# Performance work log

Measured on AMD Instinct MI355X. Metric: run time of the kernel, lower is better.

Reference implementation:

```python
import jax, jax.numpy as jnp
import numpy as np

P = 100000   # num places
T = 100000   # num transitions
E = 400000   # edges per direction
H = 128      # hidden_dim
L = 3        # num_gnn_layers


def setup_inputs() -> dict:
    key = jax.random.key(0)
    ks = jax.random.split(key, 24)
    w = lambda i, sh: jax.random.normal(ks[i], sh, dtype=jnp.float32) * 0.02
    z = lambda sh: jnp.zeros(sh, dtype=jnp.float32)
    return {
        "place_features": jax.random.uniform(ks[0], (P,), dtype=jnp.float32),
        "transition_features": jax.random.normal(ks[1], (T, 8), dtype=jnp.float32),
        "prefix_encoding": jax.random.normal(ks[2], (18,), dtype=jnp.float32),
        # pre edges: place -> transition ; post edges: transition -> place
        "pre_edge_index": jnp.stack([jax.random.randint(ks[3], (E,), 0, P),
                                     jax.random.randint(ks[4], (E,), 0, T)]).astype(jnp.int32),
        "post_edge_index": jnp.stack([jax.random.randint(ks[5], (E,), 0, T),
                                      jax.random.randint(ks[6], (E,), 0, P)]).astype(jnp.int32),
        # embeddings
        "W_pe": w(7, (1, H)), "b_pe": z((H,)),
        "W_te": w(8, (8, H)), "b_te": z((H,)),
        "W_pr": w(9, (18, H)), "b_pr": z((H,)),
        # per-layer HeteroGraphConv params (stacked over L)
        "p2t_W": w(10, (L, H, H)), "p2t_b": z((L, H)),
        "t2p_W": w(11, (L, H, H)), "t2p_b": z((L, H)),
        "pu_W": w(12, (L, 2 * H, H)), "pu_b": z((L, H)),
        "tu_W": w(13, (L, 2 * H, H)), "tu_b": z((L, H)),
        "pa_W": w(14, (L, H)), "pa_b": z((L,)),
        "ta_W": w(15, (L, H)), "ta_b": z((L,)),
        # pooling + predictor head
        "W_pp": w(16, (H, H)), "b_pp": z((H,)),
        "W_tp": w(17, (H, H)), "b_tp": z((H,)),
        "W1": w(18, (3 * H, 2 * H)), "b1": z((2 * H,)),
        "W2": w(19, (2 * H, H)), "b2": z((H,)),
        "W3": w(20, (H, T)), "b3": z((T,)),
    }


def _forward(place_features, transition_features, prefix_encoding,
             W_pe, b_pe, W_te, b_te, W_pr, b_pr,
             p2t_W, p2t_b, t2p_W, t2p_b, pu_W, pu_b, tu_W, tu_b,
             pa_W, pa_b, ta_W, ta_b,
             W_pp, b_pp, W_tp, b_tp, W1, b1, W2, b2, W3, b3,
             pre_edge_index, post_edge_index):
    place_h = place_features[:, None] @ W_pe + b_pe            # [P,H]
    trans_h = transition_features @ W_te + b_te                # [T,H]
    prefix_h = prefix_encoding[None, :] @ W_pr + b_pr          # [1,H]
    p_src, p_dst = pre_edge_index[0], pre_edge_index[1]        # place idx, trans idx
    t_src, t_dst = post_edge_index[0], post_edge_index[1]      # trans idx, place idx
    nP, nT = place_h.shape[0], trans_h.shape[0]
    for l in range(L):  # fixed small layer count
        # place -> transition: gather, linear, softmax over ALL edges (dim=0 in torch), scatter-add
        m_pt = place_h[p_src] @ p2t_W[l] + p2t_b[l]            # [E,H]
        a_pt = jax.nn.softmax(m_pt @ ta_W[l] + ta_b[l], axis=0)  # [E]
        trans_msg = jax.ops.segment_sum(m_pt * a_pt[:, None], p_dst, num_segments=nT)
        # transition -> place
        m_tp = trans_h[t_src] @ t2p_W[l] + t2p_b[l]            # [E,H]
        a_tp = jax.nn.softmax(m_tp @ pa_W[l] + pa_b[l], axis=0)
        place_msg = jax.ops.segment_sum(m_tp * a_tp[:, None], t_dst, num_segments=nP)
        # residual update + relu (dropout is identity at eval)
        place_new = jnp.concatenate([place_h, place_msg], axis=1) @ pu_W[l] + pu_b[l]
        trans_new = jnp.concatenate([trans_h, trans_msg], axis=1) @ tu_W[l] + tu_b[l]
        place_h = jax.nn.relu(place_h + place_new)
        trans_h = jax.nn.relu(trans_h + trans_new)
    place_global = jnp.mean(place_h @ W_pp + b_pp, axis=0, keepdims=True)   # [1,H]
    trans_global = jnp.mean(trans_h @ W_tp + b_tp, axis=0, keepdims=True)   # [1,H]
    combined = jnp.concatenate([place_global, trans_global, prefix_h], axis=1)  # [1,3H]
    h1 = jax.nn.relu(combined @ W1 + b1)
    h2 = jax.nn.relu(h1 @ W2 + b2)
    logits = h2 @ W3 + b3                                      # [1,T]
    return jax.nn.sigmoid(logits)                              # predicted_transitions


def reference(place_features, transition_features, prefix_encoding,
              pre_edge_index, post_edge_index,
              W_pe, b_pe, W_te, b_te, W_pr, b_pr,
              p2t_W, p2t_b, t2p_W, t2p_b, pu_W, pu_b, tu_W, tu_b,
              pa_W, pa_b, ta_W, ta_b,
              W_pp, b_pp, W_tp, b_tp, W1, b1, W2, b2, W3, b3):
    return _forward(place_features, transition_features, prefix_encoding,
                    W_pe, b_pe, W_te, b_te, W_pr, b_pr,
                    p2t_W, p2t_b, t2p_W, t2p_b, pu_W, pu_b, tu_W, tu_b,
                    pa_W, pa_b, ta_W, ta_b,
                    W_pp, b_pp, W_tp, b_tp, W1, b1, W2, b2, W3, b3,
                    pre_edge_index, post_edge_index)
```

## Files before the change

### kernel.cpp

```cpp
#include <hip/hip_runtime.h>
#include <cstddef>

#define H 128

typedef unsigned short ushort_t;
typedef unsigned char uchar_t;
typedef __attribute__((ext_vector_type(8))) short short8;
typedef __attribute__((ext_vector_type(4))) float floatx4;
typedef __attribute__((ext_vector_type(2))) float floatx2;

__device__ __forceinline__ unsigned fkey(float f){
    unsigned u = __float_as_uint(f);
    return (u & 0x80000000u) ? ~u : (u | 0x80000000u);
}
__device__ __forceinline__ float funkey(unsigned k){
    unsigned u = (k & 0x80000000u) ? (k ^ 0x80000000u) : ~k;
    return __uint_as_float(u);
}
__device__ __forceinline__ ushort_t f2bf(float f){
    unsigned u = __float_as_uint(f);
    u += 0x7fffu + ((u >> 16) & 1u);
    return (ushort_t)(u >> 16);
}
__device__ __forceinline__ float bf2f(ushort_t h){
    return __uint_as_float(((unsigned)h) << 16);
}
__device__ __forceinline__ uchar_t f2fp8(float v){
    int p = __builtin_amdgcn_cvt_pk_fp8_f32(v, v, 0, false);
    return (uchar_t)(p & 0xff);
}
__device__ __forceinline__ void gll16(const void* g, void* l){
    __builtin_amdgcn_global_load_lds(
        (const __attribute__((address_space(1))) unsigned int*)g,
        (__attribute__((address_space(3))) unsigned int*)l, 16, 0, 0);
}

__global__ __launch_bounds__(256) void k_embed_place(
    const float* __restrict__ pf, const float* __restrict__ Wpe,
    const float* __restrict__ bpe, ushort_t* __restrict__ out, int P)
{
    int idx = blockIdx.x*256 + threadIdx.x;
    if (idx >= P*32) return;
    int p = idx >> 5, q = (idx & 31) << 2;
    float v = pf[p];
    float4 w = *(const float4*)(Wpe + q);
    float4 b = *(const float4*)(bpe + q);
    ushort4 o;
    o.x = f2bf(v*w.x + b.x); o.y = f2bf(v*w.y + b.y);
    o.z = f2bf(v*w.z + b.z); o.w = f2bf(v*w.w + b.w);
    *(ushort4*)(out + (size_t)p*H + q) = o;
}

__global__ __launch_bounds__(256) void k_embed_trans(
    const float* __restrict__ tf, const float* __restrict__ Wte,
    const float* __restrict__ bte, ushort_t* __restrict__ out, int T)
{
    __shared__ float Wl[8*H];
    __shared__ float Bl[H];
    int tid = threadIdx.x;
    #pragma unroll
    for (int t = 0; t < 4; t++) Wl[tid + t*256] = Wte[tid + t*256];
    if (tid < H) Bl[tid] = bte[tid];
    __syncthreads();
    int idx = blockIdx.x*256 + tid;
    if (idx >= T*32) return;
    int t = idx >> 5, q = (idx & 31) << 2;
    float4 acc = *(float4*)(&Bl[q]);
    #pragma unroll
    for (int k = 0; k < 8; k++){
        float s = tf[(size_t)t*8 + k];
        float4 w = *(float4*)(&Wl[k*H + q]);
        acc.x += s*w.x; acc.y += s*w.y; acc.z += s*w.z; acc.w += s*w.w;
    }
    ushort4 o;
    o.x = f2bf(acc.x); o.y = f2bf(acc.y); o.z = f2bf(acc.z); o.w = f2bf(acc.w);
    *(ushort4*)(out + (size_t)t*H + q) = o;
}

__global__ void k_init_small(const float* __restrict__ pe, int plen,
                             const float* __restrict__ Wpr, const float* __restrict__ bpr,
                             float* __restrict__ prefix, float* __restrict__ meanP,
                             float* __restrict__ meanT, float* __restrict__ slots)
{
    int c = threadIdx.x;
    float a = bpr[c];
    for (int k = 0; k < plen; k++) a += pe[k]*Wpr[k*H + c];
    prefix[c] = a;
    meanP[c] = 0.f;
    meanT[c] = 0.f;
    if (c < 16) slots[c] = 0.f;
}

__global__ __launch_bounds__(256) void k_wconv(
    const float* __restrict__ p2t_W, const float* __restrict__ t2p_W,
    const float* __restrict__ tu_W,  const float* __restrict__ pu_W,
    ushort_t* __restrict__ WT, int total)
{
    int e = blockIdx.x*256 + threadIdx.x;
    if (e >= total) return;
    int l = e / 98304, o = e - l*98304;
    const float* src; int K, oo;
    if (o < 16384)      { src = p2t_W + (size_t)l*16384; K = 128; oo = o; }
    else if (o < 32768) { src = t2p_W + (size_t)l*16384; K = 128; oo = o - 16384; }
    else if (o < 65536) { src = tu_W  + (size_t)l*32768; K = 256; oo = o - 32768; }
    else                { src = pu_W  + (size_t)l*32768; K = 256; oo = o - 65536; }
    int n = oo / K, k = oo - n*K;
    WT[e] = f2bf(src[(size_t)k*H + n]);
}

__global__ __launch_bounds__(256) void k_zero_ints(int* __restrict__ p, int n)
{
    int i = blockIdx.x*256 + threadIdx.x;
    int stride = gridDim.x*256;
    for (; i < n; i += stride) p[i] = 0;
}

__global__ __launch_bounds__(256) void k_hist2(
    const int* __restrict__ preD, const int* __restrict__ postD, int E,
    int* __restrict__ cntPre, int* __restrict__ cntPost,
    int* __restrict__ rankPre, int* __restrict__ rankPost)
{
    int i = blockIdx.x*256 + threadIdx.x;
    int stride = gridDim.x*256;
    for (; i < E; i += stride){
        rankPre[i] = atomicAdd(&cntPre[preD[i]], 1);
        rankPost[i] = atomicAdd(&cntPost[postD[i]], 1);
    }
}

__global__ __launch_bounds__(256) void k_scan_part(
    const int* __restrict__ cnt, int N, int* __restrict__ bsum)
{
    __shared__ int wsum[4];
    int tid = threadIdx.x, lane = tid & 63, wid = tid >> 6;
    int base = blockIdx.x*1024 + tid*4;
    int4 v = make_int4(0,0,0,0);
    if (base + 3 < N) v = *(const int4*)(cnt + base);
    else {
        if (base+0 < N) v.x = cnt[base+0];
        if (base+1 < N) v.y = cnt[base+1];
        if (base+2 < N) v.z = cnt[base+2];
    }
    int s = v.x + v.y + v.z + v.w;
    #pragma unroll
    for (int o = 1; o < 64; o <<= 1) s += __shfl_xor(s, o);
    if (lane == 0) wsum[wid] = s;
    __syncthreads();
    if (tid == 0) bsum[blockIdx.x] = wsum[0] + wsum[1] + wsum[2] + wsum[3];
}

__global__ __launch_bounds__(256) void k_scan_bsum(int* __restrict__ bsum, int nb)
{
    __shared__ int wsum[4];
    int tid = threadIdx.x, lane = tid & 63, wid = tid >> 6;
    int x = (tid < nb) ? bsum[tid] : 0;
    int inc = x;
    #pragma unroll
    for (int o = 1; o < 64; o <<= 1){
        int u = __shfl_up(inc, o);
        if (lane >= o) inc += u;
    }
    if (lane == 63) wsum[wid] = inc;
    __syncthreads();
    int woff = 0;
    if (wid > 0) woff += wsum[0];
    if (wid > 1) woff += wsum[1];
    if (wid > 2) woff += wsum[2];
    if (tid < nb) bsum[tid] = woff + inc - x;
}

__global__ __launch_bounds__(256) void k_scan_final(
    const int* __restrict__ cnt, int N, const int* __restrict__ bsum,
    int* __restrict__ rp, int E)
{
    __shared__ int wsum[4];
    int tid = threadIdx.x, lane = tid & 63, wid = tid >> 6;
    int base = blockIdx.x*1024 + tid*4;
    int4 v = make_int4(0,0,0,0);
    if (base + 3 < N) v = *(const int4*)(cnt + base);
    else {
        if (base+0 < N) v.x = cnt[base+0];
        if (base+1 < N) v.y = cnt[base+1];
        if (base+2 < N) v.z = cnt[base+2];
    }
    int t0 = v.x, t1 = t0 + v.y, t2 = t1 + v.z, t3 = t2 + v.w;
    int inc = t3;
    #pragma unroll
    for (int o = 1; o < 64; o <<= 1){
        int u = __shfl_up(inc, o);
        if (lane >= o) inc += u;
    }
    if (lane == 63) wsum[wid] = inc;
    __syncthreads();
    int woff = 0;
    if (wid > 0) woff += wsum[0];
    if (wid > 1) woff += wsum[1];
    if (wid > 2) woff += wsum[2];
    int off = bsum[blockIdx.x] + woff + inc - t3;
    if (base+0 < N) rp[base+0] = off;
    if (base+1 < N) rp[base+1] = off + t0;
    if (base+2 < N) rp[base+2] = off + t1;
    if (base+3 < N) rp[base+3] = off + t2;
    if (blockIdx.x == 0 && tid == 0) rp[N] = E;
}

__global__ __launch_bounds__(256) void k_fill2(
    const int* __restrict__ preS, const int* __restrict__ preD,
    const int* __restrict__ postS, const int* __restrict__ postD, int E,
    const int* __restrict__ rpPre, const int* __restrict__ rankPre, int* __restrict__ csrPre,
    const int* __restrict__ rpPost, const int* __restrict__ rankPost, int* __restrict__ csrPost)
{
    int i = blockIdx.x*256 + threadIdx.x;
    int stride = gridDim.x*256;
    for (; i < E; i += stride){
        csrPre[rpPre[preD[i]] + rankPre[i]] = preS[i];
        csrPost[rpPost[postD[i]] + rankPost[i]] = postS[i];
    }
}

__global__ __launch_bounds__(256, 4) void k_gemm_msg(
    const ushort_t* __restrict__ A, const ushort_t* __restrict__ WT,
    const float* __restrict__ bias, uchar_t* __restrict__ out, int M,
    const float* __restrict__ aw, float* __restrict__ y4)
{
    __shared__ __align__(16) char As[3*4096];
    int tid = threadIdx.x;
    int lane = tid & 63, wid = tid >> 6;
    int quad = lane >> 4, l15 = lane & 15;
    int strip = wid*32;
    short8 bfr[2][4];
    float bcol[2], awc[2];
    #pragma unroll
    for (int j = 0; j < 2; j++){
        int col = strip + j*16 + l15;
        #pragma unroll
        for (int kk = 0; kk < 4; kk++)
            bfr[j][kk] = *(const short8*)(WT + (size_t)col*128 + kk*32 + quad*8);
        bcol[j] = bias[col];
        awc[j]  = aw[col];
    }
    int tiles = (M + 15) >> 4;
    int G = gridDim.x;
    int t0 = blockIdx.x;
    if (t0 >= tiles) return;

    int srow = tid >> 4;
    int su = (tid & 15) ^ srow;
    const ushort_t* gb = A + (size_t)srow*H + su*8;
    char* AsB = As;

    #define STAGE_MSG(bo, t) gll16(gb + (size_t)(t)*(16*H), AsB + (bo) + (wid<<10))

    STAGE_MSG(0, t0);
    int t1p = t0 + G;
    if (t1p < tiles){
        STAGE_MSG(4096, t1p);
        asm volatile("s_waitcnt vmcnt(1)\ns_barrier" ::: "memory");
    } else {
        asm volatile("s_waitcnt vmcnt(0)\ns_barrier" ::: "memory");
    }

    int t = t0, bo = 0;
    for (;;){
        const char* rb = AsB + bo;
        short8 afr[4];
        #pragma unroll
        for (int kk = 0; kk < 4; kk++)
            afr[kk] = *(const short8*)(rb + (l15<<8) + ((((kk<<2)+quad) ^ l15) << 4));
        floatx4 acc[2];
        acc[0] = (floatx4)0.f; acc[1] = (floatx4)0.f;
        #pragma unroll
        for (int j = 0; j < 2; j++)
            #pragma unroll
            for (int kk = 0; kk < 4; kk++)
                acc[j] = __builtin_amdgcn_mfma_f32_16x16x32_bf16(afr[kk], bfr[j][kk], acc[j], 0,0,0);
        int row0 = t << 4;
        float pr[4] = {0.f,0.f,0.f,0.f};
        #pragma unroll
        for (int j = 0; j < 2; j++){
            int col = strip + j*16 + l15;
            #pragma unroll
            for (int rr = 0; rr < 4; rr++){
                int grow = row0 + quad*4 + rr;
                float v = acc[j][rr] + bcol[j];
                out[(size_t)grow*H + col] = f2fp8(v);
                pr[rr] += v * awc[j];
            }
        }
        #pragma unroll
        for (int rr = 0; rr < 4; rr++){
            float p = pr[rr];
            p += __shfl_xor(p, 1); p += __shfl_xor(p, 2);
            p += __shfl_xor(p, 4); p += __shfl_xor(p, 8);
            int grow = row0 + quad*4 + rr;
            if (l15 == 0) y4[(size_t)grow*4 + wid] = p;
        }
        int tn = t + G;
        if (tn >= tiles) break;
        int tnn = tn + G;
        int bo2 = bo + 4096; if (bo2 >= 12288) bo2 = 0;
        int bo3 = bo2 + 4096; if (bo3 >= 12288) bo3 = 0;
        if (tnn < tiles){
            STAGE_MSG(bo3, tnn);
            asm volatile("s_waitcnt vmcnt(13)\ns_barrier" ::: "memory");
        } else {
            asm volatile("s_waitcnt vmcnt(12)\ns_barrier" ::: "memory");
        }
        t = tn; bo = bo2;
    }
    #undef STAGE_MSG
}

__global__ __launch_bounds__(256) void k_scoremax(
    const float* __restrict__ y4, int N, const float* __restrict__ abp,
    float* __restrict__ y, unsigned* __restrict__ Mkey)
{
    __shared__ float wm[4];
    int tid = threadIdx.x;
    int lane = tid & 63, wid = tid >> 6;
    int gid = blockIdx.x*256 + tid, stride = gridDim.x*256;
    float ab = abp[0];
    float lmax = -3.402823466e38f;
    for (int r = gid; r < N; r += stride){
        float4 v = *(const float4*)(y4 + (size_t)r*4);
        float s = v.x + v.y + v.z + v.w + ab;
        y[r] = s;
        lmax = fmaxf(lmax, s);
    }
    #pragma unroll
    for (int o = 1; o < 64; o <<= 1) lmax = fmaxf(lmax, __shfl_xor(lmax, o));
    if (lane == 0) wm[wid] = lmax;
    __syncthreads();
    if (tid == 0){
        float m = fmaxf(fmaxf(wm[0], wm[1]), fmaxf(wm[2], wm[3]));
        atomicMax(Mkey, fkey(m));
    }
}

__global__ __launch_bounds__(256) void k_sumexp(
    const int* __restrict__ src, int E, const float* __restrict__ y,
    const unsigned* __restrict__ Mkey, float* __restrict__ Sp)
{
    __shared__ float red[4];
    int tid = threadIdx.x, lane = tid & 63, wid = tid >> 6;
    int gid = blockIdx.x*256 + tid, stride = gridDim.x*256;
    float Mv = funkey(Mkey[0]);
    float ls = 0.f;
    for (int e = gid; e < E; e += stride) ls += expf(y[src[e]] - Mv);
    #pragma unroll
    for (int o = 1; o < 64; o <<= 1) ls += __shfl_xor(ls, o);
    if (lane == 0) red[wid] = ls;
    __syncthreads();
    if (tid == 0) atomicAdd(Sp, red[0] + red[1] + red[2] + red[3]);
}

__global__ __launch_bounds__(256, 3) void k_gemm_up(
    const ushort_t* __restrict__ A1, const ushort_t* __restrict__ A2,
    const ushort_t* __restrict__ WT, const float* __restrict__ bias,
    const float* __restrict__ Sp, ushort_t* __restrict__ out, int M,
    float* __restrict__ colsum)
{
    __shared__ __align__(16) char As[3*8192];
    __shared__ float csum[H];
    int tid = threadIdx.x;
    int lane = tid & 63, wid = tid >> 6;
    int quad = lane >> 4, l15 = lane & 15;
    int strip = wid*32;
    short8 bfr1[2][4], bfr2[2][4];
    float bcol[2];
    #pragma unroll
    for (int j = 0; j < 2; j++){
        int col = strip + j*16 + l15;
        #pragma unroll
        for (int kk = 0; kk < 4; kk++){
            bfr1[j][kk] = *(const short8*)(WT + (size_t)col*256 + kk*32 + quad*8);
            bfr2[j][kk] = *(const short8*)(WT + (size_t)col*256 + 128 + kk*32 + quad*8);
        }
        bcol[j] = bias[col];
    }
    short8 If0, If1;
    #pragma unroll
    for (int e = 0; e < 8; e++){
        int kloc = quad*8 + e;
        If0[e] = (kloc == l15)      ? (short)0x3F80 : (short)0;
        If1[e] = (kloc == l15 + 16) ? (short)0x3F80 : (short)0;
    }
    float invS = 1.f / Sp[0];
    const bool has_cs = (colsum != nullptr);
    if (has_cs && tid < H) csum[tid] = 0.f;

    int tiles = (M + 15) >> 4;
    int G = gridDim.x;
    int t0 = blockIdx.x;
    if (t0 >= tiles) return;
    int srow = tid >> 4;
    int su = (tid & 15) ^ srow;
    const ushort_t* g1b = A1 + (size_t)srow*H + su*8;
    const ushort_t* g2b = A2 + (size_t)srow*H + su*8;
    char* AsB = As;

    #define STAGE_UP(bo, t) do { \
        gll16(g1b + (size_t)(t)*(16*H), AsB + (bo) + (wid<<10)); \
        gll16(g2b + (size_t)(t)*(16*H), AsB + (bo) + 4096 + (wid<<10)); \
    } while(0)

    STAGE_UP(0, t0);
    int t1p = t0 + G;
    if (t1p < tiles){
        STAGE_UP(8192, t1p);
        asm volatile("s_waitcnt vmcnt(2)\ns_barrier" ::: "memory");
    } else {
        asm volatile("s_waitcnt vmcnt(0)\ns_barrier" ::: "memory");
    }

    float cs[2] = {0.f, 0.f};
    int t = t0, bo = 0;
    for (;;){
        const char* rb = AsB + bo;
        short8 a1f[4], a2f[4];
        #pragma unroll
        for (int kk = 0; kk < 4; kk++){
            int sw = ((((kk<<2)+quad) ^ l15) << 4);
            a1f[kk] = *(const short8*)(rb + (l15<<8) + sw);
            a2f[kk] = *(const short8*)(rb + 4096 + (l15<<8) + sw);
        }
        short8 ares = *(const short8*)(rb + (l15<<8) + ((((wid<<2)+quad) ^ l15) << 4));
        floatx4 acc1[2], acc2[2];
        acc1[0] = __builtin_amdgcn_mfma_f32_16x16x32_bf16(ares, If0, (floatx4)0.f, 0,0,0);
        acc1[1] = __builtin_amdgcn_mfma_f32_16x16x32_bf16(ares, If1, (floatx4)0.f, 0,0,0);
        acc2[0] = (floatx4)0.f; acc2[1] = (floatx4)0.f;
        #pragma unroll
        for (int j = 0; j < 2; j++){
            #pragma unroll
            for (int kk = 0; kk < 4; kk++)
                acc1[j] = __builtin_amdgcn_mfma_f32_16x16x32_bf16(a1f[kk], bfr1[j][kk], acc1[j], 0,0,0);
            #pragma unroll
            for (int kk = 0; kk < 4; kk++)
                acc2[j] = __builtin_amdgcn_mfma_f32_16x16x32_bf16(a2f[kk], bfr2[j][kk], acc2[j], 0,0,0);
        }
        int row0 = t << 4;
        #pragma unroll
        for (int j = 0; j < 2; j++){
            int col = strip + j*16 + l15;
            #pragma unroll
            for (int rr = 0; rr < 4; rr++){
                int grow = row0 + quad*4 + rr;
                float v = acc1[j][rr] + invS*acc2[j][rr] + bcol[j];
                v = fmaxf(v, 0.f);
                out[(size_t)grow*H + col] = f2bf(v);
                if (has_cs) cs[j] += v;
            }
        }
        int tn = t + G;
        if (tn >= tiles) break;
        int tnn = tn + G;
        int bo2 = bo + 8192; if (bo2 >= 24576) bo2 = 0;
        int bo3 = bo2 + 8192; if (bo3 >= 24576) bo3 = 0;
        if (tnn < tiles){
            STAGE_UP(bo3, tnn);
            asm volatile("s_waitcnt vmcnt(10)\ns_barrier" ::: "memory");
        } else {
            asm volatile("s_waitcnt vmcnt(8)\ns_barrier" ::: "memory");
        }
        t = tn; bo = bo2;
    }
    #undef STAGE_UP
    if (has_cs){
        #pragma unroll
        for (int j = 0; j < 2; j++){
            float v = cs[j];
            v += __shfl_xor(v, 16); v += __shfl_xor(v, 32);
            if (quad == 0) atomicAdd(&csum[strip + j*16 + l15], v);
        }
        __syncthreads();
        if (tid < H) atomicAdd(&colsum[tid], csum[tid]);
    }
}

__device__ __forceinline__ void acc8f8(float* a, int2 u, float w){
    floatx2 p;
    p = __builtin_amdgcn_cvt_pk_f32_fp8(u.x, false); a[0] += w*p.x; a[1] += w*p.y;
    p = __builtin_amdgcn_cvt_pk_f32_fp8(u.x, true);  a[2] += w*p.x; a[3] += w*p.y;
    p = __builtin_amdgcn_cvt_pk_f32_fp8(u.y, false); a[4] += w*p.x; a[5] += w*p.y;
    p = __builtin_amdgcn_cvt_pk_f32_fp8(u.y, true);  a[6] += w*p.x; a[7] += w*p.y;
}

__global__ __launch_bounds__(256) void k_gather(
    const int* __restrict__ rp, const int* __restrict__ csr, int Nrow,
    const float* __restrict__ y, const uchar_t* __restrict__ X,
    ushort_t* __restrict__ Mb, const unsigned* __restrict__ Mkey)
{
    int tid = threadIdx.x;
    int g = tid >> 4, gl = tid & 15;
    int r = blockIdx.x*16 + g;
    if (r >= Nrow) return;
    float Mv = funkey(Mkey[0]);
    int j0 = rp[r], j1 = rp[r+1];
    const int2* X8 = (const int2*)X;
    float a[8] = {0.f,0.f,0.f,0.f,0.f,0.f,0.f,0.f};
    int j = j0;
    for (; j + 1 < j1; j += 2){
        int s0 = csr[j], s1 = csr[j+1];
        float e0 = expf(y[s0] - Mv);
        float e1 = expf(y[s1] - Mv);
        int2 u0 = X8[(size_t)s0*16 + gl];
        int2 u1 = X8[(size_t)s1*16 + gl];
        acc8f8(a, u0, e0);
        acc8f8(a, u1, e1);
    }
    if (j < j1){
        int s0 = csr[j];
        float e0 = expf(y[s0] - Mv);
        int2 u0 = X8[(size_t)s0*16 + gl];
        acc8f8(a, u0, e0);
    }
    int4 o;
    o.x = (int)((((unsigned)f2bf(a[1])) << 16) | (unsigned)f2bf(a[0]));
    o.y = (int)((((unsigned)f2bf(a[3])) << 16) | (unsigned)f2bf(a[2]));
    o.z = (int)((((unsigned)f2bf(a[5])) << 16) | (unsigned)f2bf(a[4]));
    o.w = (int)((((unsigned)f2bf(a[7])) << 16) | (unsigned)f2bf(a[6]));
    ((int4*)Mb)[(size_t)r*16 + gl] = o;
}

__global__ __launch_bounds__(256) void k_head(
    const float* __restrict__ meanP, const float* __restrict__ meanT,
    float invP, float invT,
    const float* __restrict__ Wpp, const float* __restrict__ bpp,
    const float* __restrict__ Wtp, const float* __restrict__ btp,
    const float* __restrict__ prefix,
    const float* __restrict__ W1, const float* __restrict__ b1,
    const float* __restrict__ W2, const float* __restrict__ b2,
    float* __restrict__ h2g)
{
    __shared__ float comb[384];
    __shared__ float h1s[256];
    int tid = threadIdx.x;
    if (tid < 128){
        float a = bpp[tid];
        for (int k = 0; k < 128; k++) a += meanP[k]*invP*Wpp[k*H + tid];
        comb[tid] = a;
        comb[256 + tid] = prefix[tid];
    } else {
        int c = tid - 128;
        float a = btp[c];
        for (int k = 0; k < 128; k++) a += meanT[k]*invT*Wtp[k*H + c];
        comb[128 + c] = a;
    }
    __syncthreads();
    {
        float a = b1[tid];
        for (int k = 0; k < 384; k++) a += comb[k]*W1[k*256 + tid];
        h1s[tid] = fmaxf(a, 0.f);
    }
    __syncthreads();
    if (tid < 128){
        float a = b2[tid];
        for (int k = 0; k < 256; k++) a += h1s[k]*W2[k*H + tid];
        h2g[tid] = fmaxf(a, 0.f);
    }
}

__global__ __launch_bounds__(256) void k_logits(
    const float* __restrict__ h2g, const float* __restrict__ W3,
    const float* __restrict__ b3, float* __restrict__ out, int T)
{
    __shared__ float h2l[128];
    int tid = threadIdx.x;
    if (tid < 128) h2l[tid] = h2g[tid];
    __syncthreads();
    int t = blockIdx.x*256 + tid;
    if (t >= T) return;
    float a = b3[t];
    #pragma unroll 8
    for (int k = 0; k < 128; k++) a += h2l[k]*W3[(size_t)k*T + t];
    out[t] = 1.f/(1.f + expf(-a));
}

extern "C" void kernel_launch(void* const* d_in, const int* in_sizes, int n_in,
                              void* d_out, int out_size, void* d_ws, size_t ws_size,
                              hipStream_t stream)
{
    (void)n_in; (void)out_size; (void)ws_size;
    const float* pf    = (const float*)d_in[0];
    const float* tf    = (const float*)d_in[1];
    const float* pe    = (const float*)d_in[2];
    const int*   pre   = (const int*)d_in[3];
    const int*   post  = (const int*)d_in[4];
    const float* W_pe  = (const float*)d_in[5];
    const float* b_pe  = (const float*)d_in[6];
    const float* W_te  = (const float*)d_in[7];
    const float* b_te  = (const float*)d_in[8];
    const float* W_pr  = (const float*)d_in[9];
    const float* b_pr  = (const float*)d_in[10];
    const float* p2t_W = (const float*)d_in[11];
    const float* p2t_b = (const float*)d_in[12];
    const float* t2p_W = (const float*)d_in[13];
    const float* t2p_b = (const float*)d_in[14];
    const float* pu_W  = (const float*)d_in[15];
    const float* pu_b  = (const float*)d_in[16];
    const float* tu_W  = (const float*)d_in[17];
    const float* tu_b  = (const float*)d_in[18];
    const float* pa_W  = (const float*)d_in[19];
    const float* pa_b  = (const float*)d_in[20];
    const float* ta_W  = (const float*)d_in[21];
    const float* ta_b  = (const float*)d_in[22];
    const float* W_pp  = (const float*)d_in[23];
    const float* b_pp  = (const float*)d_in[24];
    const float* W_tp  = (const float*)d_in[25];
    const float* b_tp  = (const float*)d_in[26];
    const float* W1    = (const float*)d_in[27];
    const float* b1    = (const float*)d_in[28];
    const float* W2    = (const float*)d_in[29];
    const float* b2    = (const float*)d_in[30];
    const float* W3    = (const float*)d_in[31];
    const float* b3    = (const float*)d_in[32];

    int P = in_sizes[0];
    int T = in_sizes[1] / 8;
    int E = in_sizes[3] / 2;
    int plen = in_sizes[2];
    int L = in_sizes[11] / (H*H);

    float* ws = (float*)d_ws;
    size_t fP = (size_t)P*H, fT = (size_t)T*H;
    size_t fN = (fP > fT) ? fP : fT;
    int   Nmax = (P > T) ? P : T;

    float* yb = ws;
    float* y4 = yb + Nmax;
    float* sc = y4 + (size_t)Nmax*4;
    float* meanP   = sc + 16;
    float* meanT   = sc + 144;
    float* prefix  = sc + 272;
    float* h2g     = sc + 400;

    ushort_t* bh = (ushort_t*)(sc + 544);
    ushort_t* place_h = bh;
    ushort_t* trans_h = place_h + fP;
    ushort_t* Mb      = trans_h + fT;
    ushort_t* Pb2     = Mb + fN;
    ushort_t* Tb2     = Pb2 + fP;
    ushort_t* WTb     = Tb2 + fT;
    uchar_t*  Xf8     = (uchar_t*)(WTb + (size_t)L*98304);

    int* iw = (int*)(Xf8 + fN);
    int* cntPre  = iw;
    int* cntPost = cntPre + T;
    int* rpPre   = cntPost + P;
    int* rpPost  = rpPre + (T + 1);
    int* csrPre  = rpPost + (P + 2);
    int* csrPost = csrPre + E;
    int* rankPre = csrPost + E;
    int* rankPost= rankPre + E;
    int* bsumA   = rankPost + E;
    int* bsumB   = bsumA + 256;

    const int* pre_src  = pre;          const int* pre_dst  = pre + E;
    const int* post_src = post;         const int* post_dst = post + E;

    int wtot = L*98304;
    int nbT = (T + 1023)/1024, nbP = (P + 1023)/1024;

    int gemmGrid = 1250;

    k_init_small<<<1, 128, 0, stream>>>(pe, plen, W_pr, b_pr, prefix, meanP, meanT, sc);
    k_wconv<<<(wtot + 255)/256, 256, 0, stream>>>(p2t_W, t2p_W, tu_W, pu_W, WTb, wtot);
    k_zero_ints<<<256, 256, 0, stream>>>(iw, P + T);
    k_hist2<<<2048, 256, 0, stream>>>(pre_dst, post_dst, E,
                                      cntPre, cntPost, rankPre, rankPost);
    k_scan_part<<<nbT, 256, 0, stream>>>(cntPre, T, bsumA);
    k_scan_bsum<<<1, 256, 0, stream>>>(bsumA, nbT);
    k_scan_final<<<nbT, 256, 0, stream>>>(cntPre, T, bsumA, rpPre, E);
    k_scan_part<<<nbP, 256, 0, stream>>>(cntPost, P, bsumB);
    k_scan_bsum<<<1, 256, 0, stream>>>(bsumB, nbP);
    k_scan_final<<<nbP, 256, 0, stream>>>(cntPost, P, bsumB, rpPost, E);
    k_fill2<<<1024, 256, 0, stream>>>(pre_src, pre_dst, post_src, post_dst, E,
                                      rpPre, rankPre, csrPre,
                                      rpPost, rankPost, csrPost);

    k_embed_place<<<(P*32 + 255)/256, 256, 0, stream>>>(pf, W_pe, b_pe, place_h, P);
    k_embed_trans<<<(T*32 + 255)/256, 256, 0, stream>>>(tf, W_te, b_te, trans_h, T);

    ushort_t* curP = place_h; ushort_t* altP = Pb2;
    ushort_t* curT = trans_h; ushort_t* altT = Tb2;

    for (int l = 0; l < L; l++){
        const ushort_t* WTl  = WTb + (size_t)l*98304;
        const ushort_t* p2tT = WTl;
        const ushort_t* t2pT = WTl + 16384;
        const ushort_t* tuT  = WTl + 32768;
        const ushort_t* puT  = WTl + 65536;
        const float* p2tb = p2t_b + (size_t)l*H;
        const float* t2pb = t2p_b + (size_t)l*H;
        const float* pub  = pu_b  + (size_t)l*H;
        const float* tub  = tu_b  + (size_t)l*H;
        const float* paW  = pa_W + (size_t)l*H;   const float* pab = pa_b + l;
        const float* taW  = ta_W + (size_t)l*H;   const float* tab = ta_b + l;
        unsigned* MkA = (unsigned*)(sc + l*4 + 0);   float* SpA = sc + l*4 + 1;
        unsigned* MkB = (unsigned*)(sc + l*4 + 2);   float* SpB = sc + l*4 + 3;
        int last = (l == L-1);

        k_gemm_msg<<<gemmGrid, 256, 0, stream>>>(curP, p2tT, p2tb, Xf8, P, taW, y4);
        k_scoremax<<<128, 256, 0, stream>>>(y4, P, tab, yb, MkA);
        k_sumexp<<<256, 256, 0, stream>>>(pre_src, E, yb, MkA, SpA);
        k_gather<<<(T + 15)/16, 256, 0, stream>>>(rpPre, csrPre, T, yb, Xf8, Mb, MkA);

        k_gemm_msg<<<gemmGrid, 256, 0, stream>>>(curT, t2pT, t2pb, Xf8, T, paW, y4);
        k_scoremax<<<128, 256, 0, stream>>>(y4, T, pab, yb, MkB);
        k_sumexp<<<256, 256, 0, stream>>>(post_src, E, yb, MkB, SpB);

        k_gemm_up<<<gemmGrid, 256, 0, stream>>>(curT, Mb, tuT, tub, SpA, altT, T,
                                                last ? meanT : nullptr);

        k_gather<<<(P + 15)/16, 256, 0, stream>>>(rpPost, csrPost, P, yb, Xf8, Mb, MkB);
        k_gemm_up<<<gemmGrid, 256, 0, stream>>>(curP, Mb, puT, pub, SpB, altP, P,
                                                last ? meanP : nullptr);

        ushort_t* tmp;
        tmp = curT; curT = altT; altT = tmp;
        tmp = curP; curP = altP; altP = tmp;
    }

    k_head<<<1, 256, 0, stream>>>(meanP, meanT, 1.f/(float)P, 1.f/(float)T,
                                  W_pp, b_pp, W_tp, b_tp, prefix, W1, b1, W2, b2, h2g);
    k_logits<<<(T + 255)/256, 256, 0, stream>>>(h2g, W3, b3, (float*)d_out, T);
}
```

Before: 731.0 us.

## Fold message projection into update weights and replace message GEMM with GEMV

```diff
diff --git a/kernel.cpp b/kernel.cpp
--- a/kernel.cpp
+++ b/kernel.cpp
@@ -7,7 +7,6 @@
 typedef unsigned char uchar_t;
 typedef __attribute__((ext_vector_type(8))) short short8;
 typedef __attribute__((ext_vector_type(4))) float floatx4;
-typedef __attribute__((ext_vector_type(2))) float floatx2;
 
 __device__ __forceinline__ unsigned fkey(float f){
     unsigned u = __float_as_uint(f);
@@ -25,14 +24,16 @@
 __device__ __forceinline__ float bf2f(ushort_t h){
     return __uint_as_float(((unsigned)h) << 16);
 }
-__device__ __forceinline__ uchar_t f2fp8(float v){
-    int p = __builtin_amdgcn_cvt_pk_fp8_f32(v, v, 0, false);
-    return (uchar_t)(p & 0xff);
-}
 __device__ __forceinline__ void gll16(const void* g, void* l){
     __builtin_amdgcn_global_load_lds(
         (const __attribute__((address_space(1))) unsigned int*)g,
         (__attribute__((address_space(3))) unsigned int*)l, 16, 0, 0);
+}
+__device__ __forceinline__ void acc8bf(float* a, int4 u, float w){
+    a[0] += w*bf2f((ushort_t)(u.x & 0xffff)); a[1] += w*bf2f((ushort_t)(((unsigned)u.x) >> 16));
+    a[2] += w*bf2f((ushort_t)(u.y & 0xffff)); a[3] += w*bf2f((ushort_t)(((unsigned)u.y) >> 16));
+    a[4] += w*bf2f((ushort_t)(u.z & 0xffff)); a[5] += w*bf2f((ushort_t)(((unsigned)u.z) >> 16));
+    a[6] += w*bf2f((ushort_t)(u.w & 0xffff)); a[7] += w*bf2f((ushort_t)(((unsigned)u.w) >> 16));
 }
 
 __global__ __launch_bounds__(256) void k_embed_place(
@@ -92,20 +93,59 @@
 }
 
 __global__ __launch_bounds__(256) void k_wconv(
+    const float* __restrict__ tu_W, const float* __restrict__ pu_W,
+    ushort_t* __restrict__ WT, int total)
+{
+    int e = blockIdx.x*256 + threadIdx.x;
+    if (e >= total) return;
+    int l = e / 32768, oo = e - l*32768;
+    int side = oo >> 14, o2 = oo & 16383;
+    int n = o2 >> 7, k = o2 & 127;
+    const float* Bm = side ? (pu_W + (size_t)l*32768) : (tu_W + (size_t)l*32768);
+    WT[(size_t)l*65536 + (size_t)side*32768 + n*256 + k] = f2bf(Bm[(size_t)k*H + n]);
+}
+
+__global__ __launch_bounds__(256) void k_wprep(
     const float* __restrict__ p2t_W, const float* __restrict__ t2p_W,
     const float* __restrict__ tu_W,  const float* __restrict__ pu_W,
-    ushort_t* __restrict__ WT, int total)
-{
-    int e = blockIdx.x*256 + threadIdx.x;
-    if (e >= total) return;
-    int l = e / 98304, o = e - l*98304;
-    const float* src; int K, oo;
-    if (o < 16384)      { src = p2t_W + (size_t)l*16384; K = 128; oo = o; }
-    else if (o < 32768) { src = t2p_W + (size_t)l*16384; K = 128; oo = o - 16384; }
-    else if (o < 65536) { src = tu_W  + (size_t)l*32768; K = 256; oo = o - 32768; }
-    else                { src = pu_W  + (size_t)l*32768; K = 256; oo = o - 65536; }
-    int n = oo / K, k = oo - n*K;
-    WT[e] = f2bf(src[(size_t)k*H + n]);
+    const float* __restrict__ p2t_b, const float* __restrict__ t2p_b,
+    const float* __restrict__ ta_W,  const float* __restrict__ ta_b,
+    const float* __restrict__ pa_W,  const float* __restrict__ pa_b,
+    ushort_t* __restrict__ WT, float* __restrict__ wv,
+    float* __restrict__ c0v, float* __restrict__ bcv)
+{
+    int b = blockIdx.x;
+    int l = b >> 3, sub = b & 7;
+    int side = sub >> 2, q = sub & 3;
+    const float* A  = side ? (t2p_W + (size_t)l*16384) : (p2t_W + (size_t)l*16384);
+    const float* Bm = side ? (pu_W  + (size_t)l*32768) : (tu_W  + (size_t)l*32768);
+    const float* ab = side ? (t2p_b + (size_t)l*H) : (p2t_b + (size_t)l*H);
+    const float* av = side ? (pa_W  + (size_t)l*H) : (ta_W  + (size_t)l*H);
+    float asc       = side ? pa_b[l] : ta_b[l];
+    int tid = threadIdx.x;
+    ushort_t* Wdst = WT + (size_t)l*65536 + (size_t)side*32768;
+    for (int idx = q*4096 + tid; idx < (q+1)*4096; idx += 256){
+        int n = idx >> 7, k = idx & 127;
+        float s = 0.f;
+        for (int j = 0; j < 128; j++) s += A[(size_t)k*H + j] * Bm[(size_t)(128+j)*H + n];
+        Wdst[(size_t)n*256 + 128 + k] = f2bf(s);
+    }
+    if (q == 0){
+        int o = (l*2 + side)*H;
+        if (tid < H){
+            float s = 0.f;
+            for (int n = 0; n < 128; n++) s += A[(size_t)tid*H + n] * av[n];
+            wv[o + tid] = s;
+            float s2 = 0.f;
+            for (int j = 0; j < 128; j++) s2 += ab[j] * Bm[(size_t)(128+j)*H + tid];
+            bcv[o + tid] = s2;
+        }
+        if (tid == 0){
+            float s = 0.f;
+            for (int n = 0; n < 128; n++) s += ab[n]*av[n];
+            c0v[l*2 + side] = s + asc;
+        }
+    }
 }
 
 __global__ __launch_bounds__(256) void k_zero_ints(int* __restrict__ p, int n)
@@ -218,113 +258,29 @@
     }
 }
 
-__global__ __launch_bounds__(256, 4) void k_gemm_msg(
-    const ushort_t* __restrict__ A, const ushort_t* __restrict__ WT,
-    const float* __restrict__ bias, uchar_t* __restrict__ out, int M,
-    const float* __restrict__ aw, float* __restrict__ y4)
-{
-    __shared__ __align__(16) char As[3*4096];
-    int tid = threadIdx.x;
-    int lane = tid & 63, wid = tid >> 6;
-    int quad = lane >> 4, l15 = lane & 15;
-    int strip = wid*32;
-    short8 bfr[2][4];
-    float bcol[2], awc[2];
-    #pragma unroll
-    for (int j = 0; j < 2; j++){
-        int col = strip + j*16 + l15;
+__global__ __launch_bounds__(256) void k_gemv(
+    const ushort_t* __restrict__ A, int M,
+    const float* __restrict__ wv, const float* __restrict__ c0v, int c0i,
+    float* __restrict__ y, unsigned* __restrict__ Mkey)
+{
+    __shared__ float wm[4];
+    int tid = threadIdx.x, lane = tid & 63, wid = tid >> 6;
+    int g = tid >> 4, gl = tid & 15;
+    float w8[8];
+    #pragma unroll
+    for (int i = 0; i < 8; i++) w8[i] = wv[gl*8 + i];
+    float c0 = c0v[c0i];
+    int stride = gridDim.x*16;
+    float lmax = -3.402823466e38f;
+    for (int r = blockIdx.x*16 + g; r < M; r += stride){
+        short8 u = *(const short8*)(A + (size_t)r*H + gl*8);
+        float s = 0.f;
         #pragma unroll
-        for (int kk = 0; kk < 4; kk++)
-            bfr[j][kk] = *(const short8*)(WT + (size_t)col*128 + kk*32 + quad*8);
-        bcol[j] = bias[col];
-        awc[j]  = aw[col];
-    }
-    int tiles = (M + 15) >> 4;
-    int G = gridDim.x;
-    int t0 = blockIdx.x;
-    if (t0 >= tiles) return;
-
-    int srow = tid >> 4;
-    int su = (tid & 15) ^ srow;
-    const ushort_t* gb = A + (size_t)srow*H + su*8;
-    char* AsB = As;
-
-    #define STAGE_MSG(bo, t) gll16(gb + (size_t)(t)*(16*H), AsB + (bo) + (wid<<10))
-
-    STAGE_MSG(0, t0);
-    int t1p = t0 + G;
-    if (t1p < tiles){
-        STAGE_MSG(4096, t1p);
-        asm volatile("s_waitcnt vmcnt(1)\ns_barrier" ::: "memory");
-    } else {
-        asm volatile("s_waitcnt vmcnt(0)\ns_barrier" ::: "memory");
-    }
-
-    int t = t0, bo = 0;
-    for (;;){
-        const char* rb = AsB + bo;
-        short8 afr[4];
-        #pragma unroll
-        for (int kk = 0; kk < 4; kk++)
-            afr[kk] = *(const short8*)(rb + (l15<<8) + ((((kk<<2)+quad) ^ l15) << 4));
-        floatx4 acc[2];
-        acc[0] = (floatx4)0.f; acc[1] = (floatx4)0.f;
-        #pragma unroll
-        for (int j = 0; j < 2; j++)
-            #pragma unroll
-            for (int kk = 0; kk < 4; kk++)
-                acc[j] = __builtin_amdgcn_mfma_f32_16x16x32_bf16(afr[kk], bfr[j][kk], acc[j], 0,0,0);
-        int row0 = t << 4;
-        float pr[4] = {0.f,0.f,0.f,0.f};
-        #pragma unroll
-        for (int j = 0; j < 2; j++){
-            int col = strip + j*16 + l15;
-            #pragma unroll
-            for (int rr = 0; rr < 4; rr++){
-                int grow = row0 + quad*4 + rr;
-                float v = acc[j][rr] + bcol[j];
-                out[(size_t)grow*H + col] = f2fp8(v);
-                pr[rr] += v * awc[j];
-            }
-        }
-        #pragma unroll
-        for (int rr = 0; rr < 4; rr++){
-            float p = pr[rr];
-            p += __shfl_xor(p, 1); p += __shfl_xor(p, 2);
-            p += __shfl_xor(p, 4); p += __shfl_xor(p, 8);
-            int grow = row0 + quad*4 + rr;
-            if (l15 == 0) y4[(size_t)grow*4 + wid] = p;
-        }
-        int tn = t + G;
-        if (tn >= tiles) break;
-        int tnn = tn + G;
-        int bo2 = bo + 4096; if (bo2 >= 12288) bo2 = 0;
-        int bo3 = bo2 + 4096; if (bo3 >= 12288) bo3 = 0;
-        if (tnn < tiles){
-            STAGE_MSG(bo3, tnn);
-            asm volatile("s_waitcnt vmcnt(13)\ns_barrier" ::: "memory");
-        } else {
-            asm volatile("s_waitcnt vmcnt(12)\ns_barrier" ::: "memory");
-        }
-        t = tn; bo = bo2;
-    }
-    #undef STAGE_MSG
-}
-
-__global__ __launch_bounds__(256) void k_scoremax(
-    const float* __restrict__ y4, int N, const float* __restrict__ abp,
-    float* __restrict__ y, unsigned* __restrict__ Mkey)
-{
-    __shared__ float wm[4];
-    int tid = threadIdx.x;
-    int lane = tid & 63, wid = tid >> 6;
-    int gid = blockIdx.x*256 + tid, stride = gridDim.x*256;
-    float ab = abp[0];
-    float lmax = -3.402823466e38f;
-    for (int r = gid; r < N; r += stride){
-        float4 v = *(const float4*)(y4 + (size_t)r*4);
-        float s = v.x + v.y + v.z + v.w + ab;
-        y[r] = s;
+        for (int i = 0; i < 8; i++) s += bf2f((ushort_t)u[i]) * w8[i];
+        s += __shfl_xor(s, 1); s += __shfl_xor(s, 2);
+        s += __shfl_xor(s, 4); s += __shfl_xor(s, 8);
+        s += c0;
+        if (gl == 0) y[r] = s;
         lmax = fmaxf(lmax, s);
     }
     #pragma unroll
@@ -354,11 +310,54 @@
     if (tid == 0) atomicAdd(Sp, red[0] + red[1] + red[2] + red[3]);
 }
 
-__global__ __launch_bounds__(256, 3) void k_gemm_up(
+__global__ __launch_bounds__(256) void k_gatherH(
+    const int* __restrict__ rp, const int* __restrict__ csr, int Nrow,
+    const float* __restrict__ y, const ushort_t* __restrict__ Hsrc,
+    ushort_t* __restrict__ G, float* __restrict__ sdeg,
+    const unsigned* __restrict__ Mkey)
+{
+    int tid = threadIdx.x;
+    int g = tid >> 4, gl = tid & 15;
+    int r = blockIdx.x*16 + g;
+    if (r >= Nrow) return;
+    float Mv = funkey(Mkey[0]);
+    int j0 = rp[r], j1 = rp[r+1];
+    const int4* H4 = (const int4*)Hsrc;
+    float a[8] = {0.f,0.f,0.f,0.f,0.f,0.f,0.f,0.f};
+    float se = 0.f;
+    int j = j0;
+    for (; j + 1 < j1; j += 2){
+        int s0 = csr[j], s1 = csr[j+1];
+        float e0 = expf(y[s0] - Mv);
+        float e1 = expf(y[s1] - Mv);
+        int4 u0 = H4[(size_t)s0*16 + gl];
+        int4 u1 = H4[(size_t)s1*16 + gl];
+        se += e0 + e1;
+        acc8bf(a, u0, e0);
+        acc8bf(a, u1, e1);
+    }
+    if (j < j1){
+        int s0 = csr[j];
+        float e0 = expf(y[s0] - Mv);
+        int4 u0 = H4[(size_t)s0*16 + gl];
+        se += e0;
+        acc8bf(a, u0, e0);
+    }
+    int4 o;
+    o.x = (int)((((unsigned)f2bf(a[1])) << 16) | (unsigned)f2bf(a[0]));
+    o.y = (int)((((unsigned)f2bf(a[3])) << 16) | (unsigned)f2bf(a[2]));
+    o.z = (int)((((unsigned)f2bf(a[5])) << 16) | (unsigned)f2bf(a[4]));
+    o.w = (int)((((unsigned)f2bf(a[7])) << 16) | (unsigned)f2bf(a[6]));
+    ((int4*)G)[(size_t)r*16 + gl] = o;
+    if (gl == 0) sdeg[r] = se;
+}
+
+__global__ __launch_bounds__(256, 4) void k_gemm_up(
     const ushort_t* __restrict__ A1, const ushort_t* __restrict__ A2,
     const ushort_t* __restrict__ WT, const float* __restrict__ bias,
-    const float* __restrict__ Sp, ushort_t* __restrict__ out, int M,
-    float* __restrict__ colsum)
+    const float* __restrict__ bcp, const float* __restrict__ Sp,
+    const float* __restrict__ sdeg,
+    ushort_t* __restrict__ out, int M, float* __restrict__ colsum)
 {
     __shared__ __align__(16) char As[3*8192];
     __shared__ float csum[H];
@@ -367,7 +366,7 @@
     int quad = lane >> 4, l15 = lane & 15;
     int strip = wid*32;
     short8 bfr1[2][4], bfr2[2][4];
-    float bcol[2];
+    float bcol[2], bc2[2];
     #pragma unroll
     for (int j = 0; j < 2; j++){
         int col = strip + j*16 + l15;
@@ -377,6 +376,7 @@
             bfr2[j][kk] = *(const short8*)(WT + (size_t)col*256 + 128 + kk*32 + quad*8);
         }
         bcol[j] = bias[col];
+        bc2[j]  = bcp[col];
     }
     short8 If0, If1;
     #pragma unroll
@@ -388,6 +388,7 @@
     float invS = 1.f / Sp[0];
     const bool has_cs = (colsum != nullptr);
     if (has_cs && tid < H) csum[tid] = 0.f;
+    float cs[2] = {0.f, 0.f};
 
     int tiles = (M + 15) >> 4;
     int G = gridDim.x;
@@ -413,10 +414,12 @@
         asm volatile("s_waitcnt vmcnt(0)\ns_barrier" ::: "memory");
     }
 
-    float cs[2] = {0.f, 0.f};
     int t = t0, bo = 0;
     for (;;){
         const char* rb = AsB + bo;
+        int row0 = t << 4;
+        float4 sd4 = *(const float4*)(sdeg + row0 + quad*4);
+        float sdv[4] = {sd4.x, sd4.y, sd4.z, sd4.w};
         short8 a1f[4], a2f[4];
         #pragma unroll
         for (int kk = 0; kk < 4; kk++){
@@ -438,14 +441,13 @@
             for (int kk = 0; kk < 4; kk++)
                 acc2[j] = __builtin_amdgcn_mfma_f32_16x16x32_bf16(a2f[kk], bfr2[j][kk], acc2[j], 0,0,0);
         }
-        int row0 = t << 4;
         #pragma unroll
         for (int j = 0; j < 2; j++){
             int col = strip + j*16 + l15;
             #pragma unroll
             for (int rr = 0; rr < 4; rr++){
                 int grow = row0 + quad*4 + rr;
-                float v = acc1[j][rr] + invS*acc2[j][rr] + bcol[j];
+                float v = acc1[j][rr] + invS*(acc2[j][rr] + sdv[rr]*bc2[j]) + bcol[j];
                 v = fmaxf(v, 0.f);
                 out[(size_t)grow*H + col] = f2bf(v);
                 if (has_cs) cs[j] += v;
@@ -458,9 +460,9 @@
         int bo3 = bo2 + 8192; if (bo3 >= 24576) bo3 = 0;
         if (tnn < tiles){
             STAGE_UP(bo3, tnn);
-            asm volatile("s_waitcnt vmcnt(10)\ns_barrier" ::: "memory");
+            asm volatile("s_waitcnt vmcnt(11)\ns_barrier" ::: "memory");
         } else {
-            asm volatile("s_waitcnt vmcnt(8)\ns_barrier" ::: "memory");
+            asm volatile("s_waitcnt vmcnt(9)\ns_barrier" ::: "memory");
         }
         t = tn; bo = bo2;
     }
@@ -475,51 +477,6 @@
         __syncthreads();
         if (tid < H) atomicAdd(&colsum[tid], csum[tid]);
     }
-}
-
-__device__ __forceinline__ void acc8f8(float* a, int2 u, float w){
-    floatx2 p;
-    p = __builtin_amdgcn_cvt_pk_f32_fp8(u.x, false); a[0] += w*p.x; a[1] += w*p.y;
-    p = __builtin_amdgcn_cvt_pk_f32_fp8(u.x, true);  a[2] += w*p.x; a[3] += w*p.y;
-    p = __builtin_amdgcn_cvt_pk_f32_fp8(u.y, false); a[4] += w*p.x; a[5] += w*p.y;
-    p = __builtin_amdgcn_cvt_pk_f32_fp8(u.y, true);  a[6] += w*p.x; a[7] += w*p.y;
-}
-
-__global__ __launch_bounds__(256) void k_gather(
-    const int* __restrict__ rp, const int* __restrict__ csr, int Nrow,
-    const float* __restrict__ y, const uchar_t* __restrict__ X,
-    ushort_t* __restrict__ Mb, const unsigned* __restrict__ Mkey)
-{
-    int tid = threadIdx.x;
-    int g = tid >> 4, gl = tid & 15;
-    int r = blockIdx.x*16 + g;
-    if (r >= Nrow) return;
-    float Mv = funkey(Mkey[0]);
-    int j0 = rp[r], j1 = rp[r+1];
-    const int2* X8 = (const int2*)X;
-    float a[8] = {0.f,0.f,0.f,0.f,0.f,0.f,0.f,0.f};
-    int j = j0;
-    for (; j + 1 < j1; j += 2){
-        int s0 = csr[j], s1 = csr[j+1];
-        float e0 = expf(y[s0] - Mv);
-        float e1 = expf(y[s1] - Mv);
-        int2 u0 = X8[(size_t)s0*16 + gl];
-        int2 u1 = X8[(size_t)s1*16 + gl];
-        acc8f8(a, u0, e0);
-        acc8f8(a, u1, e1);
-    }
-    if (j < j1){
-        int s0 = csr[j];
-        float e0 = expf(y[s0] - Mv);
-        int2 u0 = X8[(size_t)s0*16 + gl];
-        acc8f8(a, u0, e0);
-    }
-    int4 o;
-    o.x = (int)((((unsigned)f2bf(a[1])) << 16) | (unsigned)f2bf(a[0]));
-    o.y = (int)((((unsigned)f2bf(a[3])) << 16) | (unsigned)f2bf(a[2]));
-    o.z = (int)((((unsigned)f2bf(a[5])) << 16) | (unsigned)f2bf(a[4]));
-    o.w = (int)((((unsigned)f2bf(a[7])) << 16) | (unsigned)f2bf(a[6]));
-    ((int4*)Mb)[(size_t)r*16 + gl] = o;
 }
 
 __global__ __launch_bounds__(256) void k_head(
@@ -626,24 +583,26 @@
     size_t fN = (fP > fT) ? fP : fT;
     int   Nmax = (P > T) ? P : T;
 
-    float* yb = ws;
-    float* y4 = yb + Nmax;
-    float* sc = y4 + (size_t)Nmax*4;
+    float* yb   = ws;
+    float* sdeg = yb + Nmax;
+    float* sc   = sdeg + Nmax;
     float* meanP   = sc + 16;
     float* meanT   = sc + 144;
     float* prefix  = sc + 272;
     float* h2g     = sc + 400;
-
-    ushort_t* bh = (ushort_t*)(sc + 544);
+    float* wvv  = sc + 544;
+    float* c0v  = wvv + (size_t)L*256;
+    float* bcv  = c0v + 32;
+
+    ushort_t* bh = (ushort_t*)(bcv + (size_t)L*256);
     ushort_t* place_h = bh;
     ushort_t* trans_h = place_h + fP;
-    ushort_t* Mb      = trans_h + fT;
-    ushort_t* Pb2     = Mb + fN;
+    ushort_t* Gb      = trans_h + fT;
+    ushort_t* Pb2     = Gb + fN;
     ushort_t* Tb2     = Pb2 + fP;
     ushort_t* WTb     = Tb2 + fT;
-    uchar_t*  Xf8     = (uchar_t*)(WTb + (size_t)L*98304);
-
-    int* iw = (int*)(Xf8 + fN);
+
+    int* iw = (int*)(WTb + (size_t)L*65536);
     int* cntPre  = iw;
     int* cntPost = cntPre + T;
     int* rpPre   = cntPost + P;
@@ -658,13 +617,16 @@
     const int* pre_src  = pre;          const int* pre_dst  = pre + E;
     const int* post_src = post;         const int* post_dst = post + E;
 
-    int wtot = L*98304;
+    int wtot = L*32768;
     int nbT = (T + 1023)/1024, nbP = (P + 1023)/1024;
 
-    int gemmGrid = 1250;
+    int tilesP = (P + 15) >> 4, tilesT = (T + 15) >> 4;
+    int gridP = (tilesP + 4)/5, gridT = (tilesT + 4)/5;
 
     k_init_small<<<1, 128, 0, stream>>>(pe, plen, W_pr, b_pr, prefix, meanP, meanT, sc);
-    k_wconv<<<(wtot + 255)/256, 256, 0, stream>>>(p2t_W, t2p_W, tu_W, pu_W, WTb, wtot);
+    k_wconv<<<(wtot + 255)/256, 256, 0, stream>>>(tu_W, pu_W, WTb, wtot);
+    k_wprep<<<L*8, 256, 0, stream>>>(p2t_W, t2p_W, tu_W, pu_W, p2t_b, t2p_b,
+                                     ta_W, ta_b, pa_W, pa_b, WTb, wvv, c0v, bcv);
     k_zero_ints<<<256, 256, 0, stream>>>(iw, P + T);
     k_hist2<<<2048, 256, 0, stream>>>(pre_dst, post_dst, E,
                                       cntPre, cntPost, rankPre, rankPost);
@@ -685,36 +647,33 @@
     ushort_t* curT = trans_h; ushort_t* altT = Tb2;
 
     for (int l = 0; l < L; l++){
-        const ushort_t* WTl  = WTb + (size_t)l*98304;
-        const ushort_t* p2tT = WTl;
-        const ushort_t* t2pT = WTl + 16384;
-        const ushort_t* tuT  = WTl + 32768;
-        const ushort_t* puT  = WTl + 65536;
-        const float* p2tb = p2t_b + (size_t)l*H;
-        const float* t2pb = t2p_b + (size_t)l*H;
+        const ushort_t* tuT = WTb + (size_t)l*65536;
+        const ushort_t* puT = tuT + 32768;
         const float* pub  = pu_b  + (size_t)l*H;
         const float* tub  = tu_b  + (size_t)l*H;
-        const float* paW  = pa_W + (size_t)l*H;   const float* pab = pa_b + l;
-        const float* taW  = ta_W + (size_t)l*H;   const float* tab = ta_b + l;
+        const float* wvA  = wvv + (size_t)(l*2 + 0)*H;
+        const float* wvB  = wvv + (size_t)(l*2 + 1)*H;
+        const float* bcA  = bcv + (size_t)(l*2 + 0)*H;
+        const float* bcB  = bcv + (size_t)(l*2 + 1)*H;
         unsigned* MkA = (unsigned*)(sc + l*4 + 0);   float* SpA = sc + l*4 + 1;
         unsigned* MkB = (unsigned*)(sc + l*4 + 2);   float* SpB = sc + l*4 + 3;
         int last = (l == L-1);
 
-        k_gemm_msg<<<gemmGrid, 256, 0, stream>>>(curP, p2tT, p2tb, Xf8, P, taW, y4);
-        k_scoremax<<<128, 256, 0, stream>>>(y4, P, tab, yb, MkA);
+        k_gemv<<<512, 256, 0, stream>>>(curP, P, wvA, c0v, l*2 + 0, yb, MkA);
         k_sumexp<<<256, 256, 0, stream>>>(pre_src, E, yb, MkA, SpA);
-        k_gather<<<(T + 15)/16, 256, 0, stream>>>(rpPre, csrPre, T, yb, Xf8, Mb, MkA);
-
-        k_gemm_msg<<<gemmGrid, 256, 0, stream>>>(curT, t2pT, t2pb, Xf8, T, paW, y4);
-        k_scoremax<<<128, 256, 0, stream>>>(y4, T, pab, yb, MkB);
+        k_gatherH<<<(T + 15)/16, 256, 0, stream>>>(rpPre, csrPre, T, yb, curP,
+                                                   Gb, sdeg, MkA);
+
+        k_gemv<<<512, 256, 0, stream>>>(curT, T, wvB, c0v, l*2 + 1, yb, MkB);
         k_sumexp<<<256, 256, 0, stream>>>(post_src, E, yb, MkB, SpB);
 
-        k_gemm_up<<<gemmGrid, 256, 0, stream>>>(curT, Mb, tuT, tub, SpA, altT, T,
-                                                last ? meanT : nullptr);
-
-        k_gather<<<(P + 15)/16, 256, 0, stream>>>(rpPost, csrPost, P, yb, Xf8, Mb, MkB);
-        k_gemm_up<<<gemmGrid, 256, 0, stream>>>(curP, Mb, puT, pub, SpB, altP, P,
-                                                last ? meanP : nullptr);
+        k_gemm_up<<<gridT, 256, 0, stream>>>(curT, Gb, tuT, tub, bcA, SpA, sdeg,
+                                             altT, T, last ? meanT : nullptr);
+
+        k_gatherH<<<(P + 15)/16, 256, 0, stream>>>(rpPost, csrPost, P, yb, curT,
+                                                   Gb, sdeg, MkB);
+        k_gemm_up<<<gridP, 256, 0, stream>>>(curP, Gb, puT, pub, bcB, SpB, sdeg,
+                                             altP, P, last ? meanP : nullptr);
 
         ushort_t* tmp;
         tmp = curT; curT = altT; altT = tmp;
```

Result: slower. 820.6 us (+12.3%).
